# Performance work log

Hardware: AMD Instinct MI355X
Metric: run time of the kernel (lower is better)

The kernel has to match this reference:

```python
import jax, jax.numpy as jnp
import numpy as np

B, H, W = 16, 32, 32
N = H * W
C_SEARCH, C_XCORR = 256, 64
C = C_SEARCH + C_XCORR          # phi_in_channels = gcn_in_channels
PHI_H = 64
GC_HID, GC_OUT = 128, 1
K_PTS = 48                       # keypoints per image
BN_EPS = 1e-5


def _build_coords_pair():
    # 8-neighbourhood pairs (distance^2 in {1,2}), exactly gen_8neigh_coords_pair
    idx = np.arange(N).reshape(H, W)
    ys, xs = np.meshgrid(np.arange(H), np.arange(W), indexing='ij')
    pairs8 = []
    for dy in (-1, 0, 1):
        for dx in (-1, 0, 1):
            if dy == 0 and dx == 0:
                continue
            ny, nx = ys + dy, xs + dx
            m = (ny >= 0) & (ny < H) & (nx >= 0) & (nx < W)
            pairs8.append(np.stack([idx[ys[m], xs[m]], idx[ny[m], nx[m]]], axis=1))
    pairs8 = np.concatenate(pairs8, 0)  # [7812, 2]
    # keypoint permutation pairs; keypoints on even coords -> disjoint from 8-neigh
    even = np.arange(0, H, 2)
    grid_idx = (even[:, None] * W + even[None, :]).reshape(-1)
    rng = np.random.default_rng(0)
    out = []
    for _ in range(B):
        kp = rng.choice(grid_idx, size=K_PTS, replace=False)
        a, b = np.meshgrid(kp, kp, indexing='ij')
        m = a != b
        kpairs = np.stack([a[m], b[m]], axis=1)  # K*(K-1) ordered pairs
        out.append(np.concatenate([kpairs, pairs8], 0))
    return np.stack(out, 0).astype(np.int32)  # [B, E, 2]


def setup_inputs() -> dict:
    key = jax.random.key(0)
    ks = jax.random.split(key, 10)
    u = lambda k, shape, s: jax.random.uniform(k, shape, jnp.float32, -s, s)
    inp = {
        'search_feature': jax.random.normal(ks[0], (B, C_SEARCH, H, W), jnp.float32),
        'xcorr_map': jax.random.normal(ks[1], (B, C_XCORR, H, W), jnp.float32),
        'coords_pair': jnp.asarray(_build_coords_pair()),
        # phi: Linear(C, PHI_H) + BN + ReLU, then Linear(PHI_H, 1) + Sigmoid
        'phi_w1': u(ks[2], (C, PHI_H), 1.0 / np.sqrt(C)),
        'phi_b1': u(ks[3], (PHI_H,), 1.0 / np.sqrt(C)),
        'bn_gamma': jnp.ones((PHI_H,), jnp.float32),
        'bn_beta': jnp.zeros((PHI_H,), jnp.float32),
        'phi_w2': u(ks[4], (PHI_H, 1), 1.0 / np.sqrt(PHI_H)),
        'phi_b2': u(ks[5], (1,), 1.0 / np.sqrt(PHI_H)),
        # GCN weights, torch init: uniform(-1/sqrt(out), 1/sqrt(out))
        'gc1_w': u(ks[6], (C, GC_HID), 1.0 / np.sqrt(GC_HID)),
        'gc2_w': u(ks[7], (GC_HID, GC_OUT), 1.0 / np.sqrt(GC_OUT)),
    }
    return inp


def reference(search_feature, xcorr_map, coords_pair, phi_w1, phi_b1,
              bn_gamma, bn_beta, phi_w2, phi_b2, gc1_w, gc2_w):
    # catted feature flattened: [B, C, N] (row-major h*W+w, matches torch view)
    feat = jnp.concatenate([search_feature, xcorr_map], axis=1).reshape(B, C, N)

    def per_image(f, pairs):  # f: [C, N], pairs: [E, 2]
        diff = jnp.abs(f[:, pairs[:, 0]] - f[:, pairs[:, 1]]).T  # [E, C]
        h = diff @ phi_w1 + phi_b1                                # [E, PHI_H]
        mu = jnp.mean(h, axis=0)
        var = jnp.var(h, axis=0)  # biased, as torch BN training mode
        h = (h - mu) / jnp.sqrt(var + BN_EPS) * bn_gamma + bn_beta
        h = jax.nn.relu(h)
        edge = jax.nn.sigmoid(h @ phi_w2 + phi_b2)[:, 0]          # [E]
        adj = jnp.zeros((N, N), jnp.float32).at[pairs[:, 0], pairs[:, 1]].set(edge)
        return adj

    adj = jax.vmap(per_image)(feat, coords_pair)  # [B, N, N]

    node_feat = feat.transpose(0, 2, 1)  # [B, N, C] (gcn_process_feat_xcorr=True)
    h = jax.nn.leaky_relu(jnp.einsum('bnm,bmd->bnd', adj, node_feat @ gc1_w), 0.2)
    mask = jax.nn.sigmoid(jnp.einsum('bnm,bmd->bnd', adj, h @ gc2_w))  # [B, N, 1]
    return mask[:, :, 0].reshape(B, 1, H, W)
```

## Files before the change

### kernel.cpp

```cpp
#include <hip/hip_runtime.h>
#include <hip/hip_bf16.h>

#define BB 16
#define NN 1024
#define CS 256
#define CX 64
#define CC 320
#define PH 64
#define GH 128
#define ELLW 64
#define NENG 7812
#define ROWP 324
#define RSTR 100

typedef __hip_bfloat16 bf16;
typedef __attribute__((ext_vector_type(8))) __bf16 bfrag;
typedef __attribute__((ext_vector_type(4))) float v4f;

__global__ __launch_bounds__(256) void k_prep(
    const float* __restrict__ w1, const float* __restrict__ gc1w,
    __bf16* __restrict__ whi, __bf16* __restrict__ wlo,
    __bf16* __restrict__ gwhi, __bf16* __restrict__ gwlo,
    int* __restrict__ cnt, float* __restrict__ Ssum, float* __restrict__ S2sum)
{
    int idx = blockIdx.x * 256 + threadIdx.x;
    if (idx < 10 * 4 * 64 * 8) {
        int j    = idx & 7;
        int lane = (idx >> 3) & 63;
        int nt   = (idx >> 9) & 3;
        int ks   = idx >> 11;
        int k = ks * 32 + (lane >> 4) * 8 + j;
        int n = nt * 16 + (lane & 15);
        float w = w1[k * PH + n];
        __bf16 h = (__bf16)w;
        whi[idx] = h;
        wlo[idx] = (__bf16)(w - (float)h);
    }
    if (idx < 10 * 8 * 64 * 8) {
        int j    = idx & 7;
        int lane = (idx >> 3) & 63;
        int nt   = (idx >> 9) & 7;
        int ks   = idx >> 12;
        int k = ks * 32 + (lane >> 4) * 8 + j;
        int n = nt * 16 + (lane & 15);
        float w = gc1w[k * GH + n];
        __bf16 h = (__bf16)w;
        gwhi[idx] = h;
        gwlo[idx] = (__bf16)(w - (float)h);
    }
    if (idx < BB * NN) cnt[idx] = 0;
    if (idx < BB * PH) { Ssum[idx] = 0.f; S2sum[idx] = 0.f; }
}

__global__ __launch_bounds__(256) void k_transpose(
    const float* __restrict__ search, const float* __restrict__ xcorr,
    float* __restrict__ featT)
{
    __shared__ float tile[32][33];
    int blk = blockIdx.x;
    int b   = blk % BB;
    int rem = blk / BB;
    int ct  = rem >> 5;
    int ntl = rem & 31;
    int tid = threadIdx.x;
    int cl = tid >> 5, nl = tid & 31;
    const float* sb = search + (size_t)b * CS * NN;
    const float* xb = xcorr + (size_t)b * CX * NN;
    #pragma unroll
    for (int f = 0; f < 4; ++f) {
        int c = ct * 32 + cl + f * 8;
        int n = ntl * 32 + nl;
        float v = (c < CS) ? sb[(size_t)c * NN + n] : xb[(size_t)(c - CS) * NN + n];
        tile[cl + f * 8][nl] = v;
    }
    __syncthreads();
    #pragma unroll
    for (int f = 0; f < 4; ++f) {
        int nr = cl + f * 8;
        int cc = nl;
        featT[((size_t)b * NN + ntl * 32 + nr) * CC + ct * 32 + cc] = tile[cc][nr];
    }
}

__global__ __launch_bounds__(512, 1) void k_edge(
    const float* __restrict__ featT, const int* __restrict__ pairs,
    const uint4* __restrict__ wglob, const float* __restrict__ b1,
    bf16* __restrict__ hstore, float* __restrict__ Ssum,
    float* __restrict__ S2sum, int E, int EKP, int nKP)
{
    __shared__ ushort Wsh[40960];
    __shared__ float RowsBuf[48 * ROWP];
    __shared__ int kpn[48];

    int t = threadIdx.x;
    int wave = t >> 6, lane = t & 63;
    int q = lane >> 4, r = lane & 15;

    {
        uint4* dst = (uint4*)Wsh;
        #pragma unroll
        for (int k = 0; k < 10; ++k)
            dst[t + k * 512] = wglob[t + k * 512];
    }
    const bfrag* WH = (const bfrag*)Wsh;
    const bfrag* WL = (const bfrag*)(Wsh + 20480);

    float b1v[4];
    #pragma unroll
    for (int nt = 0; nt < 4; ++nt) b1v[nt] = b1[nt * 16 + r];
    float ps[4], ps2[4];
    #pragma unroll
    for (int nt = 0; nt < 4; ++nt) { ps[nt] = 0.f; ps2[nt] = 0.f; }
    int b;

    if (blockIdx.x < nKP) {
        b = blockIdx.x % BB;
        int e0 = (blockIdx.x / BB) * 128;
        if (t < 48) kpn[t] = pairs[((size_t)b * E + t * 47) * 2];
        __syncthreads();

        {
            const float4* src = (const float4*)featT;
            #pragma unroll
            for (int k = 0; k < 8; ++k) {
                int idx = t + k * 512;
                if (idx < 48 * 80) {
                    int slot = idx / 80, c4 = idx - slot * 80;
                    float4 v = src[((size_t)b * NN + kpn[slot]) * 80 + c4];
                    *(float4*)&RowsBuf[slot * ROWP + c4 * 4] = v;
                }
            }
        }

        int eg = e0 + wave * 16 + r;
        int ec = eg < EKP ? eg : EKP - 1;
        int a = ec / 47, k = ec - a * 47;
        int y = k + (k >= a ? 1 : 0);
        const float* rI = &RowsBuf[a * ROWP + q * 8];
        const float* rJ = &RowsBuf[y * ROWP + q * 8];

        v4f acc[4];
        #pragma unroll
        for (int nt = 0; nt < 4; ++nt) acc[nt] = (v4f)0.f;

        __syncthreads();

        #pragma unroll
        for (int ks = 0; ks < 10; ++ks) {
            float4 fi0 = *(const float4*)(rI + ks * 32);
            float4 fi1 = *(const float4*)(rI + ks * 32 + 4);
            float4 fj0 = *(const float4*)(rJ + ks * 32);
            float4 fj1 = *(const float4*)(rJ + ks * 32 + 4);
            float df[8];
            df[0] = fabsf(fi0.x - fj0.x); df[1] = fabsf(fi0.y - fj0.y);
            df[2] = fabsf(fi0.z - fj0.z); df[3] = fabsf(fi0.w - fj0.w);
            df[4] = fabsf(fi1.x - fj1.x); df[5] = fabsf(fi1.y - fj1.y);
            df[6] = fabsf(fi1.z - fj1.z); df[7] = fabsf(fi1.w - fj1.w);

            bfrag ah, al;
            #pragma unroll
            for (int kk = 0; kk < 8; ++kk) {
                __bf16 h = (__bf16)df[kk];
                ah[kk] = h;
                al[kk] = (__bf16)(df[kk] - (float)h);
            }
            #pragma unroll
            for (int nt = 0; nt < 4; ++nt) {
                bfrag bh = WH[((ks * 4 + nt) << 6) + lane];
                bfrag bl = WL[((ks * 4 + nt) << 6) + lane];
                acc[nt] = __builtin_amdgcn_mfma_f32_16x16x32_bf16(ah, bh, acc[nt], 0, 0, 0);
                acc[nt] = __builtin_amdgcn_mfma_f32_16x16x32_bf16(ah, bl, acc[nt], 0, 0, 0);
                acc[nt] = __builtin_amdgcn_mfma_f32_16x16x32_bf16(al, bh, acc[nt], 0, 0, 0);
            }
        }

        #pragma unroll
        for (int reg = 0; reg < 4; ++reg) {
            int e = e0 + wave * 16 + q * 4 + reg;
            if (e < EKP) {
                bf16* hp = hstore + ((size_t)b * E + e) * PH + r;
                #pragma unroll
                for (int nt = 0; nt < 4; ++nt) {
                    float v = acc[nt][reg] + b1v[nt];
                    hp[nt * 16] = __float2bfloat16(v);
                    ps[nt] += v;
                    ps2[nt] = fmaf(v, v, ps2[nt]);
                }
            }
        }
    } else {
        int idx2 = blockIdx.x - nKP;
        b = idx2 % BB;
        int s = idx2 / BB;

        const int dyT[8] = {-1,-1,-1, 0, 0, 1, 1, 1};
        const int dxT[8] = {-1, 0, 1,-1, 1,-1, 0, 1};
        const int pfT[8] = {0, 961, 1953, 2914, 3906, 4898, 5859, 6851};

        int dy = dyT[wave], dx = dxT[wave];
        int y0 = dy < 0 ? 1 : 0;
        int x0 = dx < 0 ? 1 : 0;
        int ww = (dx == 0) ? 32 : 31;
        int pf = pfT[wave];
        int yA = 2 * s;

        const float* rowI[4];
        const float* rowJ[4];
        #pragma unroll
        for (int mt = 0; mt < 4; ++mt) {
            int x  = ((mt & 1) << 4) + r;
            int ni = (1 + (mt >> 1)) * 32 + x;
            int xj = x + dx; xj = xj < 0 ? 0 : (xj > 31 ? 31 : xj);
            int nj = (1 + (mt >> 1) + dy) * 32 + xj;
            rowI[mt] = &RowsBuf[ni * RSTR + q * 8];
            rowJ[mt] = &RowsBuf[nj * RSTR + q * 8];
        }

        v4f acc[4][4];
        #pragma unroll
        for (int mt = 0; mt < 4; ++mt)
            #pragma unroll
            for (int nt = 0; nt < 4; ++nt) acc[mt][nt] = (v4f)0.f;

        #pragma unroll
        for (int p = 0; p < 4; ++p) {
            __syncthreads();
            const int ch0 = p * 96;
            const int nf4 = (p < 3) ? 24 : 8;
            for (int u = t; u < 128 * nf4; u += 512) {
                int node = u / nf4, c4 = u - node * nf4;
                int gy = yA - 1 + (node >> 5);
                if (gy >= 0 && gy < 32) {
                    int gn = gy * 32 + (node & 31);
                    float4 v = *(const float4*)&featT[((size_t)b * NN + gn) * CC
                                                      + ch0 + c4 * 4];
                    *(float4*)&RowsBuf[node * RSTR + c4 * 4] = v;
                }
            }
            __syncthreads();

            const int ksBeg = p * 3;
            const int ksEnd = (p < 3) ? ksBeg + 3 : 10;
            #pragma unroll
            for (int ks = ksBeg; ks < ksEnd; ++ks) {
                int lc = ks * 32 - ch0;
                #pragma unroll
                for (int mt = 0; mt < 4; ++mt) {
                    float4 fi0 = *(const float4*)(rowI[mt] + lc);
                    float4 fi1 = *(const float4*)(rowI[mt] + lc + 4);
                    float4 fj0 = *(const float4*)(rowJ[mt] + lc);
                    float4 fj1 = *(const float4*)(rowJ[mt] + lc + 4);
                    float df[8];
                    df[0] = fabsf(fi0.x - fj0.x); df[1] = fabsf(fi0.y - fj0.y);
                    df[2] = fabsf(fi0.z - fj0.z); df[3] = fabsf(fi0.w - fj0.w);
                    df[4] = fabsf(fi1.x - fj1.x); df[5] = fabsf(fi1.y - fj1.y);
                    df[6] = fabsf(fi1.z - fj1.z); df[7] = fabsf(fi1.w - fj1.w);

                    bfrag ah, al;
                    #pragma unroll
                    for (int kk = 0; kk < 8; ++kk) {
                        __bf16 h = (__bf16)df[kk];
                        ah[kk] = h;
                        al[kk] = (__bf16)(df[kk] - (float)h);
                    }
                    #pragma unroll
                    for (int nt = 0; nt < 4; ++nt) {
                        bfrag bh = WH[((ks * 4 + nt) << 6) + lane];
                        bfrag bl = WL[((ks * 4 + nt) << 6) + lane];
                        acc[mt][nt] = __builtin_amdgcn_mfma_f32_16x16x32_bf16(
                            ah, bh, acc[mt][nt], 0, 0, 0);
                        acc[mt][nt] = __builtin_amdgcn_mfma_f32_16x16x32_bf16(
                            ah, bl, acc[mt][nt], 0, 0, 0);
                        acc[mt][nt] = __builtin_amdgcn_mfma_f32_16x16x32_bf16(
                            al, bh, acc[mt][nt], 0, 0, 0);
                    }
                }
            }
        }

        #pragma unroll
        for (int mt = 0; mt < 4; ++mt) {
            int y = yA + (mt >> 1);
            #pragma unroll
            for (int reg = 0; reg < 4; ++reg) {
                int xi = ((mt & 1) << 4) + q * 4 + reg;
                bool valid = ((unsigned)(y + dy) < 32u) && ((unsigned)(xi + dx) < 32u);
                if (valid) {
                    int e = EKP + pf + (y - y0) * ww + (xi - x0);
                    bf16* hp = hstore + ((size_t)b * E + e) * PH + r;
                    #pragma unroll
                    for (int nt = 0; nt < 4; ++nt) {
                        float v = acc[mt][nt][reg] + b1v[nt];
                        hp[nt * 16] = __float2bfloat16(v);
                        ps[nt] += v;
                        ps2[nt] = fmaf(v, v, ps2[nt]);
                    }
                }
            }
        }
    }

    __syncthreads();
    float* sS  = RowsBuf;
    float* sS2 = RowsBuf + PH;
    if (t < PH) { sS[t] = 0.f; sS2[t] = 0.f; }
    __syncthreads();
    #pragma unroll
    for (int nt = 0; nt < 4; ++nt) {
        atomicAdd(&sS[nt * 16 + r],  ps[nt]);
        atomicAdd(&sS2[nt * 16 + r], ps2[nt]);
    }
    __syncthreads();
    if (t < PH) {
        atomicAdd(&Ssum[b * PH + t],  sS[t]);
        atomicAdd(&S2sum[b * PH + t], sS2[t]);
    }
}

__global__ __launch_bounds__(256) void k_edge_val(
    const bf16* __restrict__ hstore, const float* __restrict__ Ssum,
    const float* __restrict__ S2sum, const float* __restrict__ gamma,
    const float* __restrict__ beta, const float* __restrict__ w2,
    const float* __restrict__ b2, const int* __restrict__ pairs,
    int* __restrict__ cnt, int* __restrict__ ecol, float* __restrict__ eval_,
    int E)
{
    __shared__ float ca[PH], cb[PH];
    int b = blockIdx.x % BB;
    int e = (blockIdx.x / BB) * 256 + threadIdx.x;
    if (threadIdx.x < PH) {
        int l = threadIdx.x;
        float mu = Ssum[b * PH + l] / E;
        float var = S2sum[b * PH + l] / E - mu * mu;
        float A = rsqrtf(var + 1e-5f) * gamma[l];
        ca[l] = A;
        cb[l] = beta[l] - mu * A;
    }
    __syncthreads();
    if (e >= E) return;
    const bfrag* hp = (const bfrag*)(hstore + ((size_t)b * E + e) * PH);
    float acc = 0.f;
    #pragma unroll
    for (int l8 = 0; l8 < 8; ++l8) {
        bfrag hv = hp[l8];
        #pragma unroll
        for (int c = 0; c < 8; ++c) {
            int l = l8 * 8 + c;
            float x = fmaf((float)hv[c], ca[l], cb[l]);
            x = x > 0.f ? x : 0.f;
            acc = fmaf(x, w2[l], acc);
        }
    }
    float edge = 1.f / (1.f + __expf(-(acc + b2[0])));
    const int* cp = pairs + ((size_t)b * E + e) * 2;
    int i = cp[0], j = cp[1];
    int row = b * NN + i;
    int slot = atomicAdd(&cnt[row], 1);
    if (slot < ELLW) {
        ecol[row * ELLW + slot]  = j;
        eval_[row * ELLW + slot] = edge;
    }
}

__global__ __launch_bounds__(256, 2) void k_gc1(
    const float* __restrict__ featT, const __bf16* __restrict__ gwhi,
    const __bf16* __restrict__ gwlo, float* __restrict__ g1)
{
    __shared__ ushort WG[40960];

    int t = threadIdx.x;
    int b = blockIdx.x % BB;
    int rem = blockIdx.x / BB;
    int half = rem & 1;
    int m0 = b * NN + (rem >> 1) * 64;

    {
        uint4* dst = (uint4*)WG;
        const uint4* sh = (const uint4*)gwhi;
        const uint4* sl = (const uint4*)gwlo;
        #pragma unroll
        for (int k = 0; k < 10; ++k) {
            int u = t + k * 256;
            int chunk = u >> 6, v = u & 63;
            int ks = chunk >> 2, ntp = chunk & 3;
            int src = (ks * 8 + half * 4 + ntp) * 64 + v;
            dst[u]        = sh[src];
            dst[2560 + u] = sl[src];
        }
    }

    int wave = t >> 6, lane = t & 63;
    int q = lane >> 4, r = lane & 15;
    const float* fp = featT + (size_t)(m0 + wave * 16 + r) * CC + q * 8;

    float fa[2][8];
    auto LOADA = [&](int ks, int buf) {
        const float4* p = (const float4*)(fp + ks * 32);
        *(float4*)&fa[buf][0] = p[0];
        *(float4*)&fa[buf][4] = p[1];
    };

    v4f acc[4];
    #pragma unroll
    for (int nt = 0; nt < 4; ++nt) acc[nt] = (v4f)0.f;

    LOADA(0, 0);
    __syncthreads();

    const bfrag* WGH = (const bfrag*)WG;
    const bfrag* WGL = (const bfrag*)(WG + 20480);

    #pragma unroll
    for (int ks = 0; ks < 10; ++ks) {
        int cur = ks & 1;
        if (ks < 9) LOADA(ks + 1, cur ^ 1);
        bfrag ah, al;
        #pragma unroll
        for (int kk = 0; kk < 8; ++kk) {
            float d = fa[cur][kk];
            __bf16 h = (__bf16)d;
            ah[kk] = h;
            al[kk] = (__bf16)(d - (float)h);
        }
        #pragma unroll
        for (int nt = 0; nt < 4; ++nt) {
            bfrag bh = WGH[((ks * 4 + nt) << 6) + lane];
            bfrag bl = WGL[((ks * 4 + nt) << 6) + lane];
            acc[nt] = __builtin_amdgcn_mfma_f32_16x16x32_bf16(ah, bh, acc[nt], 0, 0, 0);
            acc[nt] = __builtin_amdgcn_mfma_f32_16x16x32_bf16(ah, bl, acc[nt], 0, 0, 0);
            acc[nt] = __builtin_amdgcn_mfma_f32_16x16x32_bf16(al, bh, acc[nt], 0, 0, 0);
        }
    }
    #pragma unroll
    for (int nt = 0; nt < 4; ++nt) {
        #pragma unroll
        for (int reg = 0; reg < 4; ++reg) {
            int m = m0 + wave * 16 + q * 4 + reg;
            g1[(size_t)m * GH + (half * 4 + nt) * 16 + r] = acc[nt][reg];
        }
    }
}

__global__ __launch_bounds__(64) void k_spmm1(
    const float* __restrict__ g1, const int* __restrict__ cnt,
    const int* __restrict__ ecol, const float* __restrict__ eval_,
    const float* __restrict__ w2g, float* __restrict__ g2)
{
    int tid = threadIdx.x;
    int b = blockIdx.x % BB;
    int node = b * NN + blockIdx.x / BB;
    float wa = w2g[2 * tid], wb = w2g[2 * tid + 1];
    int c = cnt[node];
    const int* ec = ecol + (size_t)node * ELLW;
    const float* ev = eval_ + (size_t)node * ELLW;
    const float2* g1v = (const float2*)g1;
    float aa = 0.f, ab = 0.f;
    int s = 0;
    for (; s + 4 <= c; s += 4) {
        int j0 = ec[s], j1 = ec[s + 1], j2 = ec[s + 2], j3 = ec[s + 3];
        float v0 = ev[s], v1 = ev[s + 1], v2 = ev[s + 2], v3 = ev[s + 3];
        float2 u0 = g1v[((size_t)b * NN + j0) * 64 + tid];
        float2 u1 = g1v[((size_t)b * NN + j1) * 64 + tid];
        float2 u2 = g1v[((size_t)b * NN + j2) * 64 + tid];
        float2 u3 = g1v[((size_t)b * NN + j3) * 64 + tid];
        aa = fmaf(v0, u0.x, aa); ab = fmaf(v0, u0.y, ab);
        aa = fmaf(v1, u1.x, aa); ab = fmaf(v1, u1.y, ab);
        aa = fmaf(v2, u2.x, aa); ab = fmaf(v2, u2.y, ab);
        aa = fmaf(v3, u3.x, aa); ab = fmaf(v3, u3.y, ab);
    }
    for (; s < c; ++s) {
        float2 u = g1v[((size_t)b * NN + ec[s]) * 64 + tid];
        float v = ev[s];
        aa = fmaf(v, u.x, aa); ab = fmaf(v, u.y, ab);
    }
    float h1a = aa > 0.f ? aa : 0.2f * aa;
    float h1b = ab > 0.f ? ab : 0.2f * ab;
    float p = h1a * wa + h1b * wb;
    #pragma unroll
    for (int off = 32; off >= 1; off >>= 1) p += __shfl_down(p, off, 64);
    if (tid == 0) g2[node] = p;
}

__global__ __launch_bounds__(64) void k_spmm2(
    const float* __restrict__ g2, const int* __restrict__ cnt,
    const int* __restrict__ ecol, const float* __restrict__ eval_,
    float* __restrict__ out)
{
    int b = blockIdx.x % BB;
    int node = b * NN + blockIdx.x / BB;
    int lane = threadIdx.x;
    int c = cnt[node];
    float p = 0.f;
    if (lane < c) {
        int j = ecol[(size_t)node * ELLW + lane];
        p = eval_[(size_t)node * ELLW + lane] * g2[b * NN + j];
    }
    #pragma unroll
    for (int off = 32; off >= 1; off >>= 1) p += __shfl_down(p, off, 64);
    if (lane == 0) out[node] = 1.f / (1.f + __expf(-p));
}

extern "C" void kernel_launch(void* const* d_in, const int* in_sizes, int n_in,
                              void* d_out, int out_size, void* d_ws, size_t ws_size,
                              hipStream_t stream)
{
    const float* search = (const float*)d_in[0];
    const float* xcorr  = (const float*)d_in[1];
    const int*   pairs  = (const int*)d_in[2];
    const float* w1     = (const float*)d_in[3];
    const float* b1     = (const float*)d_in[4];
    const float* gamma  = (const float*)d_in[5];
    const float* beta   = (const float*)d_in[6];
    const float* w2     = (const float*)d_in[7];
    const float* b2     = (const float*)d_in[8];
    const float* gc1w   = (const float*)d_in[9];
    const float* gc2w   = (const float*)d_in[10];
    float* out = (float*)d_out;

    int E   = in_sizes[2] / (BB * 2);
    int EKP = E - NENG;
    int nb   = (E + 255) / 256;
    int nbKP = (EKP + 127) / 128;
    int nKP  = BB * nbKP;

    char* ws = (char*)d_ws;
    size_t off = 0;
    auto alloc = [&](size_t bytes) {
        size_t o = off;
        off += (bytes + 255) & ~(size_t)255;
        return o;
    };
    __bf16* whi   = (__bf16*)(ws + alloc(10 * 4 * 64 * 8 * 2));
    __bf16* wlo   = (__bf16*)(ws + alloc(10 * 4 * 64 * 8 * 2));
    __bf16* gwhi  = (__bf16*)(ws + alloc(10 * 8 * 64 * 8 * 2));
    __bf16* gwlo  = (__bf16*)(ws + alloc(10 * 8 * 64 * 8 * 2));
    float* featT  = (float*)(ws + alloc((size_t)BB * NN * CC * 4));
    bf16*  hstore = (bf16*)(ws + alloc((size_t)BB * E * PH * 2));
    float* Ssum   = (float*)(ws + alloc(BB * PH * 4));
    float* S2sum  = (float*)(ws + alloc(BB * PH * 4));
    int*   cnt    = (int*)(ws + alloc(BB * NN * 4));
    int*   ecol   = (int*)(ws + alloc((size_t)BB * NN * ELLW * 4));
    float* eval_  = (float*)(ws + alloc((size_t)BB * NN * ELLW * 4));
    float* g1     = (float*)(ws + alloc((size_t)BB * NN * GH * 4));
    float* g2     = (float*)(ws + alloc(BB * NN * 4));
    (void)ws_size; (void)n_in; (void)out_size;

    k_prep<<<dim3(160), dim3(256), 0, stream>>>(w1, gc1w, whi, wlo, gwhi, gwlo,
                                                cnt, Ssum, S2sum);
    k_transpose<<<dim3(BB * 320), dim3(256), 0, stream>>>(search, xcorr, featT);
    k_edge<<<dim3(nKP + BB * 16), dim3(512), 0, stream>>>(featT, pairs,
                                                          (const uint4*)whi, b1,
                                                          hstore, Ssum, S2sum,
                                                          E, EKP, nKP);
    k_edge_val<<<dim3(BB * nb), dim3(256), 0, stream>>>(hstore, Ssum, S2sum,
                                                        gamma, beta, w2, b2,
                                                        pairs, cnt, ecol, eval_, E);
    k_gc1<<<dim3(BB * 32), dim3(256), 0, stream>>>(featT, gwhi, gwlo, g1);
    k_spmm1<<<dim3(BB * NN), dim3(64), 0, stream>>>(g1, cnt, ecol, eval_, gc2w, g2);
    k_spmm2<<<dim3(BB * NN), dim3(64), 0, stream>>>(g2, cnt, ecol, eval_, out);
}
```

Measured before the change: 183.3 us.

## Exploit |fi-fj| symmetry to compute each unordered edge once, writing both directions

Because |f_i - f_j| is symmetric, the edge MLP's first layer output is identical for (i,j) and (j,i). Keypoint pairs are now enumerated as upper-triangle indices decoded via a sqrt-based triangular mapping, and neighbourhood edges use only 4 of 8 directions, with each result stored to both forward and reverse slots. BN partial sums are doubled accordingly and reduced with wave shuffles before the shared atomics. This roughly halves the MFMA work and block count, at the cost of a larger staging tile per block and more scattered duplicate stores.

```diff
diff --git a/kernel.cpp b/kernel.cpp
--- a/kernel.cpp
+++ b/kernel.cpp
@@ -12,10 +12,20 @@
 #define NENG 7812
 #define ROWP 324
 #define RSTR 100
+#define NKPH 1128
 
 typedef __hip_bfloat16 bf16;
 typedef __attribute__((ext_vector_type(8))) __bf16 bfrag;
 typedef __attribute__((ext_vector_type(4))) float v4f;
+
+__device__ __forceinline__ void tri_decode(int m, int& a, int& y) {
+    float s = sqrtf((float)(9025 - 8 * m));
+    int aa = (int)((95.0f - s) * 0.5f);
+    if (aa > 0 && 47 * aa - (aa * (aa - 1)) / 2 > m) --aa;
+    while (47 * (aa + 1) - ((aa + 1) * aa) / 2 <= m) ++aa;
+    a = aa;
+    y = aa + 1 + (m - (47 * aa - (aa * (aa - 1)) / 2));
+}
 
 __global__ __launch_bounds__(256) void k_prep(
     const float* __restrict__ w1, const float* __restrict__ gc1w,
@@ -89,7 +99,7 @@
     float* __restrict__ S2sum, int E, int EKP, int nKP)
 {
     __shared__ ushort Wsh[40960];
-    __shared__ float RowsBuf[48 * ROWP];
+    __shared__ float RowsBuf[16000];
     __shared__ int kpn[48];
 
     int t = threadIdx.x;
@@ -115,7 +125,7 @@
 
     if (blockIdx.x < nKP) {
         b = blockIdx.x % BB;
-        int e0 = (blockIdx.x / BB) * 128;
+        int e0h = (blockIdx.x / BB) * 128;
         if (t < 48) kpn[t] = pairs[((size_t)b * E + t * 47) * 2];
         __syncthreads();
 
@@ -132,12 +142,12 @@
             }
         }
 
-        int eg = e0 + wave * 16 + r;
-        int ec = eg < EKP ? eg : EKP - 1;
-        int a = ec / 47, k = ec - a * 47;
-        int y = k + (k >= a ? 1 : 0);
-        const float* rI = &RowsBuf[a * ROWP + q * 8];
-        const float* rJ = &RowsBuf[y * ROWP + q * 8];
+        int mA = e0h + wave * 16 + r;
+        if (mA >= NKPH) mA = NKPH - 1;
+        int aI, yI;
+        tri_decode(mA, aI, yI);
+        const float* rI = &RowsBuf[aI * ROWP + q * 8];
+        const float* rJ = &RowsBuf[yI * ROWP + q * 8];
 
         v4f acc[4];
         #pragma unroll
@@ -176,13 +186,20 @@
 
         #pragma unroll
         for (int reg = 0; reg < 4; ++reg) {
-            int e = e0 + wave * 16 + q * 4 + reg;
-            if (e < EKP) {
-                bf16* hp = hstore + ((size_t)b * E + e) * PH + r;
+            int mC = e0h + wave * 16 + q * 4 + reg;
+            if (mC < NKPH) {
+                int a, y;
+                tri_decode(mC, a, y);
+                int e1 = a * 47 + y - 1;
+                int e2 = y * 47 + a;
+                bf16* h1 = hstore + ((size_t)b * E + e1) * PH + r;
+                bf16* h2 = hstore + ((size_t)b * E + e2) * PH + r;
                 #pragma unroll
                 for (int nt = 0; nt < 4; ++nt) {
                     float v = acc[nt][reg] + b1v[nt];
-                    hp[nt * 16] = __float2bfloat16(v);
+                    bf16 vb = __float2bfloat16(v);
+                    h1[nt * 16] = vb;
+                    h2[nt * 16] = vb;
                     ps[nt] += v;
                     ps2[nt] = fmaf(v, v, ps2[nt]);
                 }
@@ -191,27 +208,31 @@
     } else {
         int idx2 = blockIdx.x - nKP;
         b = idx2 % BB;
-        int s = idx2 / BB;
-
-        const int dyT[8] = {-1,-1,-1, 0, 0, 1, 1, 1};
-        const int dxT[8] = {-1, 0, 1,-1, 1,-1, 0, 1};
-        const int pfT[8] = {0, 961, 1953, 2914, 3906, 4898, 5859, 6851};
-
-        int dy = dyT[wave], dx = dxT[wave];
+        int u = idx2 / BB;
+
+        const int dyT[4] = {-1,-1,-1, 0};
+        const int dxT[4] = {-1, 0, 1,-1};
+        const int pfT8[8] = {0, 961, 1953, 2914, 3906, 4898, 5859, 6851};
+
+        int d = wave >> 1;
+        int p = wave & 1;
+        int dy = dyT[d], dx = dxT[d];
         int y0 = dy < 0 ? 1 : 0;
         int x0 = dx < 0 ? 1 : 0;
+        int x0R = dx > 0 ? 1 : 0;
         int ww = (dx == 0) ? 32 : 31;
-        int pf = pfT[wave];
-        int yA = 2 * s;
+        int pfF = pfT8[d];
+        int pfR = pfT8[7 - d];
 
         const float* rowI[4];
         const float* rowJ[4];
         #pragma unroll
         for (int mt = 0; mt < 4; ++mt) {
             int x  = ((mt & 1) << 4) + r;
-            int ni = (1 + (mt >> 1)) * 32 + x;
+            int lr = 1 + 2 * p + (mt >> 1);
+            int ni = lr * 32 + x;
             int xj = x + dx; xj = xj < 0 ? 0 : (xj > 31 ? 31 : xj);
-            int nj = (1 + (mt >> 1) + dy) * 32 + xj;
+            int nj = (lr + dy) * 32 + xj;
             rowI[mt] = &RowsBuf[ni * RSTR + q * 8];
             rowJ[mt] = &RowsBuf[nj * RSTR + q * 8];
         }
@@ -223,14 +244,14 @@
             for (int nt = 0; nt < 4; ++nt) acc[mt][nt] = (v4f)0.f;
 
         #pragma unroll
-        for (int p = 0; p < 4; ++p) {
+        for (int ph = 0; ph < 4; ++ph) {
             __syncthreads();
-            const int ch0 = p * 96;
-            const int nf4 = (p < 3) ? 24 : 8;
-            for (int u = t; u < 128 * nf4; u += 512) {
-                int node = u / nf4, c4 = u - node * nf4;
-                int gy = yA - 1 + (node >> 5);
-                if (gy >= 0 && gy < 32) {
+            const int ch0 = ph * 96;
+            const int nf4 = (ph < 3) ? 24 : 8;
+            for (int uu = t; uu < 160 * nf4; uu += 512) {
+                int node = uu / nf4, c4 = uu - node * nf4;
+                int gy = 4 * u - 1 + (node >> 5);
+                if (gy >= 0) {
                     int gn = gy * 32 + (node & 31);
                     float4 v = *(const float4*)&featT[((size_t)b * NN + gn) * CC
                                                       + ch0 + c4 * 4];
@@ -239,8 +260,8 @@
             }
             __syncthreads();
 
-            const int ksBeg = p * 3;
-            const int ksEnd = (p < 3) ? ksBeg + 3 : 10;
+            const int ksBeg = ph * 3;
+            const int ksEnd = (ph < 3) ? ksBeg + 3 : 10;
             #pragma unroll
             for (int ks = ksBeg; ks < ksEnd; ++ks) {
                 int lc = ks * 32 - ch0;
@@ -280,18 +301,23 @@
 
         #pragma unroll
         for (int mt = 0; mt < 4; ++mt) {
-            int y = yA + (mt >> 1);
+            int y = 4 * u + 2 * p + (mt >> 1);
             #pragma unroll
             for (int reg = 0; reg < 4; ++reg) {
                 int xi = ((mt & 1) << 4) + q * 4 + reg;
-                bool valid = ((unsigned)(y + dy) < 32u) && ((unsigned)(xi + dx) < 32u);
+                int y2 = y + dy, x2 = xi + dx;
+                bool valid = ((unsigned)y2 < 32u) && ((unsigned)x2 < 32u);
                 if (valid) {
-                    int e = EKP + pf + (y - y0) * ww + (xi - x0);
-                    bf16* hp = hstore + ((size_t)b * E + e) * PH + r;
+                    int e1 = EKP + pfF + (y - y0) * ww + (xi - x0);
+                    int e2 = EKP + pfR + y2 * ww + (x2 - x0R);
+                    bf16* h1 = hstore + ((size_t)b * E + e1) * PH + r;
+                    bf16* h2 = hstore + ((size_t)b * E + e2) * PH + r;
                     #pragma unroll
                     for (int nt = 0; nt < 4; ++nt) {
                         float v = acc[mt][nt][reg] + b1v[nt];
-                        hp[nt * 16] = __float2bfloat16(v);
+                        bf16 vb = __float2bfloat16(v);
+                        h1[nt * 16] = vb;
+                        h2[nt * 16] = vb;
                         ps[nt] += v;
                         ps2[nt] = fmaf(v, v, ps2[nt]);
                     }
@@ -307,8 +333,14 @@
     __syncthreads();
     #pragma unroll
     for (int nt = 0; nt < 4; ++nt) {
-        atomicAdd(&sS[nt * 16 + r],  ps[nt]);
-        atomicAdd(&sS2[nt * 16 + r], ps2[nt]);
+        float p1 = ps[nt]  + __shfl_xor(ps[nt], 16, 64);
+        p1 += __shfl_xor(p1, 32, 64);
+        float p2 = ps2[nt] + __shfl_xor(ps2[nt], 16, 64);
+        p2 += __shfl_xor(p2, 32, 64);
+        if (lane < 16) {
+            atomicAdd(&sS[nt * 16 + r],  2.0f * p1);
+            atomicAdd(&sS2[nt * 16 + r], 2.0f * p2);
+        }
     }
     __syncthreads();
     if (t < PH) {
@@ -520,7 +552,7 @@
     int E   = in_sizes[2] / (BB * 2);
     int EKP = E - NENG;
     int nb   = (E + 255) / 256;
-    int nbKP = (EKP + 127) / 128;
+    int nbKP = (NKPH + 127) / 128;
     int nKP  = BB * nbKP;
 
     char* ws = (char*)d_ws;
@@ -548,10 +580,10 @@
     k_prep<<<dim3(160), dim3(256), 0, stream>>>(w1, gc1w, whi, wlo, gwhi, gwlo,
                                                 cnt, Ssum, S2sum);
     k_transpose<<<dim3(BB * 320), dim3(256), 0, stream>>>(search, xcorr, featT);
-    k_edge<<<dim3(nKP + BB * 16), dim3(512), 0, stream>>>(featT, pairs,
-                                                          (const uint4*)whi, b1,
-                                                          hstore, Ssum, S2sum,
-                                                          E, EKP, nKP);
+    k_edge<<<dim3(nKP + BB * 8), dim3(512), 0, stream>>>(featT, pairs,
+                                                         (const uint4*)whi, b1,
+                                                         hstore, Ssum, S2sum,
+                                                         E, EKP, nKP);
     k_edge_val<<<dim3(BB * nb), dim3(256), 0, stream>>>(hstore, Ssum, S2sum,
                                                         gamma, beta, w2, b2,
                                                         pairs, cnt, ecol, eval_, E);
```

After: 169.5 us. 1.08x faster.
